# Kernel tuning notes

Hardware: AMD Instinct MI355X
Metric: run time of the kernel (lower is better)

## Reference

```python
import jax, jax.numpy as jnp
import numpy as np


def setup_inputs() -> dict:
    key = jax.random.key(0)
    ks = jax.random.split(key, 8)
    B, N, D, H = 8, 512, 64, 64
    user_embeddings = jax.random.normal(ks[0], (B, N, D), dtype=jnp.float32)
    past_lengths = jax.random.randint(ks[1], (B,), 0, N)
    valid_mask = jnp.ones((B, N), dtype=jnp.float32)
    # MLP params: Linear(4D -> H), PReLU (single slope), Linear(H -> 1)
    s1 = 1.0 / np.sqrt(4 * D)
    s2 = 1.0 / np.sqrt(H)
    W1 = jax.random.uniform(ks[2], (H, 4 * D), minval=-s1, maxval=s1, dtype=jnp.float32)
    b1 = jax.random.uniform(ks[3], (H,), minval=-s1, maxval=s1, dtype=jnp.float32)
    prelu_a = jnp.float32(0.25)
    W2 = jax.random.uniform(ks[4], (1, H), minval=-s2, maxval=s2, dtype=jnp.float32)
    b2 = jax.random.uniform(ks[5], (1,), minval=-s2, maxval=s2, dtype=jnp.float32)
    return {"past_lengths": past_lengths, "user_embeddings": user_embeddings,
            "valid_mask": valid_mask, "W1": W1, "b1": b1, "prelu_a": prelu_a,
            "W2": W2, "b2": b2}


def reference(past_lengths, user_embeddings, valid_mask, W1, b1, prelu_a, W2, b2):
    # DIN local activation attention with causal mask.
    # Original math: h = W1 @ concat(Q, K, Q-K, Q*K) + b1 per (q,k) pair.
    # Split W1 into its 4 D-sized blocks so the concat tensor [B,N,N,4D] is
    # never materialized; the pairwise hidden [B,N,N,H] is the only big buffer.
    B, N, D = user_embeddings.shape
    Wq, Wk, Wd, Wm = jnp.split(W1, 4, axis=1)  # each [H, D]
    x = user_embeddings
    # Q and (Q-K)'s +Q part -> per-query term; K and (Q-K)'s -K part -> per-key term
    hq = jnp.einsum('bqd,hd->bqh', x, Wq + Wd)          # [B,N,H]
    hk = jnp.einsum('bkd,hd->bkh', x, Wk - Wd)          # [B,N,H]
    hm = jnp.einsum('bqd,bkd,hd->bqkh', x, x, Wm)       # [B,N,N,H] (Q*K term)
    h = hq[:, :, None, :] + hk[:, None, :, :] + hm + b1
    h = jnp.where(h > 0, h, prelu_a * h)                # PReLU
    scores = jnp.einsum('bqkh,h->bqk', h, W2[0]) + b2[0]  # [B,N,N]
    causal = jnp.tril(jnp.ones((N, N), dtype=scores.dtype))
    scores = scores * causal[None, :, :]
    scores = scores * valid_mask[:, None, :]            # key-side padding mask
    encoded = jnp.einsum('bqk,bkd->bqd', scores, x)     # weighted sum (no softmax)
    return encoded
```

## Files before the change

### kernel.cpp

```cpp
#include <hip/hip_runtime.h>

#define NB 8
#define NN 512

#define WS_WMF  0
#define WS_WQDT 4096
#define WS_WKDT 8192
#define WS_HQ   12288
#define WS_BF   274432
#define WS_XT   536576

typedef float  fx4 __attribute__((ext_vector_type(4)));
typedef short  sx8 __attribute__((ext_vector_type(8)));

static __device__ inline unsigned short f2bf(float f) {
    unsigned int u = __float_as_uint(f);
    unsigned int r = (u + 0x7FFFu + ((u >> 16) & 1u)) >> 16;
    return (unsigned short)r;
}
static __device__ inline float bfl(unsigned int u) { return __uint_as_float(u << 16); }
static __device__ inline float bfh(unsigned int u) { return __uint_as_float(u & 0xFFFF0000u); }

__global__ __launch_bounds__(256) void pkA(const float* __restrict__ W1,
                                           float* __restrict__ ws) {
    int t = threadIdx.x;
    float* wqdT = ws + WS_WQDT;
    float* wkdT = ws + WS_WKDT;
    float* wmf  = ws + WS_WMF;
    for (int i = 0; i < 16; ++i) {
        int idx = t + i * 256;
        int h = idx >> 6, d = idx & 63;
        float wq = W1[h * 256 + d];
        float wk = W1[h * 256 + 64 + d];
        float wd = W1[h * 256 + 128 + d];
        wqdT[d * 64 + h] = wq + wd;
        wkdT[d * 64 + h] = wk - wd;
    }
    for (int i = 0; i < 2; ++i) {
        int e = t + i * 256;
        int slot = e >> 6, lane = e & 63;
        int ht = slot >> 1, hf = slot & 1;
        int m = lane & 15, qd = lane >> 4;
        int h = ht * 16 + m;
        int dbase = hf * 32 + qd * 8;
        #pragma unroll
        for (int j = 0; j < 8; ++j)
            wmf[e * 8 + j] = W1[h * 256 + 192 + dbase + j];
    }
}

__global__ __launch_bounds__(256) void pkB(const float* __restrict__ x,
                                           const float* __restrict__ b1,
                                           float* __restrict__ ws) {
    const float* wqdT = ws + WS_WQDT;
    const float* wkdT = ws + WS_WKDT;
    float* hq = ws + WS_HQ;
    unsigned short* bfp = (unsigned short*)(ws + WS_BF);
    __shared__ float xs[256];
    int t = threadIdx.x;
    int r0 = blockIdx.x * 4;
    xs[t] = x[r0 * 64 + t];
    __syncthreads();
    int r = t >> 6, h = t & 63;
    const float* xr = xs + r * 64;
    float aq = b1[h], ak = 0.f;
    #pragma unroll
    for (int d = 0; d < 64; ++d) {
        float xv = xr[d];
        aq += xv * wqdT[d * 64 + h];
        ak += xv * wkdT[d * 64 + h];
    }
    int row = r0 + r;
    hq[row * 64 + h] = aq;
    int bb = row >> 9, k = row & 511;
    int tt = k >> 4, nn = k & 15;
    int c  = 2 + (h >> 5);
    int qd = (h >> 3) & 3, j = h & 7;
    int ln = qd * 16 + nn;
    bfp[((((bb * 32 + tt) * 4 + c) * 64 + ln) << 3) + j] = f2bf(ak);
}

__global__ __launch_bounds__(128) void pkC(const float* __restrict__ x,
                                           float* __restrict__ ws) {
    unsigned short* bfp = (unsigned short*)(ws + WS_BF);
    int b = blockIdx.x >> 5, t5 = blockIdx.x & 31;
    int tid = threadIdx.x;
    int c = tid >> 6, L = tid & 63;
    int nn = L & 15, qd = L >> 4;
    const float* src = x + ((b * 512 + t5 * 16 + nn) * 64 + c * 32 + qd * 8);
    fx4 v0 = *(const fx4*)src;
    fx4 v1 = *(const fx4*)(src + 4);
    uint4 o;
    o.x = (unsigned)f2bf(v0[0]) | ((unsigned)f2bf(v0[1]) << 16);
    o.y = (unsigned)f2bf(v0[2]) | ((unsigned)f2bf(v0[3]) << 16);
    o.z = (unsigned)f2bf(v1[0]) | ((unsigned)f2bf(v1[1]) << 16);
    o.w = (unsigned)f2bf(v1[2]) | ((unsigned)f2bf(v1[3]) << 16);
    *(uint4*)(bfp + ((((b * 32 + t5) * 4 + c) * 64 + L) << 3)) = o;
}

__global__ __launch_bounds__(256) void pkD(const float* __restrict__ x,
                                           const float* __restrict__ vm,
                                           float* __restrict__ ws) {
    unsigned short* xtp = (unsigned short*)(ws + WS_XT);
    int b = blockIdx.x >> 5, t5 = blockIdx.x & 31;
    int tid = threadIdx.x;
    int d = tid >> 2;
    int kl0 = (tid & 3) * 4;
    unsigned short u[4];
    #pragma unroll
    for (int i = 0; i < 4; ++i) {
        int k = t5 * 16 + kl0 + i;
        float v = x[(b * 512 + k) * 64 + d] * vm[b * 512 + k];
        u[i] = f2bf(v);
    }
    uint2 o;
    o.x = (unsigned)u[0] | ((unsigned)u[1] << 16);
    o.y = (unsigned)u[2] | ((unsigned)u[3] << 16);
    *(uint2*)(xtp + (((b * 32 + t5) * 64 + d) * 16 + kl0)) = o;
}

__global__ __launch_bounds__(256) void k2_main(const float* __restrict__ x,
                                               const float* __restrict__ prelu_a,
                                               const float* __restrict__ W2,
                                               const float* __restrict__ b2,
                                               const float* __restrict__ ws,
                                               float* __restrict__ out) {
    const int tid  = threadIdx.x;
    const int lane = tid & 63;
    const int wid  = blockIdx.x * 4 + (tid >> 6);
    const int b    = wid >> 9;
    const int rr_  = wid & 511;
    const int q    = (rr_ & 1) ? (511 - (rr_ >> 1)) : (rr_ >> 1);
    const int n    = lane & 15, quad = lane >> 4;
    const int bq   = b * 512 + q;

    const float* wmf = ws + WS_WMF;
    const float* hq  = ws + WS_HQ;
    const unsigned short* bfp = (const unsigned short*)(ws + WS_BF);
    const unsigned short* xtp = (const unsigned short*)(ws + WS_XT);

    const float pa  = prelu_a[0];
    const float b2v = b2[0];

    float hqr[4][4], w2r[4][4];
    #pragma unroll
    for (int ht = 0; ht < 4; ++ht) {
        fx4 vh = *(const fx4*)(hq + bq * 64 + ht * 16 + quad * 4);
        fx4 vw = *(const fx4*)(W2 + ht * 16 + quad * 4);
        #pragma unroll
        for (int r = 0; r < 4; ++r) { hqr[ht][r] = vh[r]; w2r[ht][r] = vw[r]; }
    }

    float xq[2][8];
    {
        const float* xp = x + bq * 64 + quad * 8;
        fx4 t0 = *(const fx4*)xp;
        fx4 t1 = *(const fx4*)(xp + 4);
        fx4 t2 = *(const fx4*)(xp + 32);
        fx4 t3 = *(const fx4*)(xp + 36);
        #pragma unroll
        for (int j = 0; j < 4; ++j) {
            xq[0][j] = t0[j]; xq[0][4 + j] = t1[j];
            xq[1][j] = t2[j]; xq[1][4 + j] = t3[j];
        }
    }

    sx8 afrag[4][2];
    #pragma unroll
    for (int ht = 0; ht < 4; ++ht)
        #pragma unroll
        for (int hf = 0; hf < 2; ++hf) {
            const float* wp = wmf + (((ht * 2 + hf) * 64 + lane) << 3);
            fx4 w0 = *(const fx4*)wp;
            fx4 w1 = *(const fx4*)(wp + 4);
            sx8 a;
            #pragma unroll
            for (int j = 0; j < 4; ++j) {
                a[j]     = (short)f2bf(w0[j] * xq[hf][j]);
                a[4 + j] = (short)f2bf(w1[j] * xq[hf][4 + j]);
            }
            afrag[ht][hf] = a;
        }

    sx8 oh[4];
    #pragma unroll
    for (int ht = 0; ht < 4; ++ht) {
        sx8 a;
        #pragma unroll
        for (int j = 0; j < 8; ++j) {
            int hp = (ht >> 1) * 32 + quad * 8 + j;
            a[j] = (hp == ht * 16 + n) ? (short)0x3F80 : (short)0;
        }
        oh[ht] = a;
    }

    float enc = 0.f;
    const int tmax = q >> 4;
    for (int t = 0; t <= tmax; ++t) {
        const unsigned short* fb = bfp + ((((b * 32 + t) * 4) * 64 + lane) << 3);
        sx8 bf0 = *(const sx8*)(fb);
        sx8 bf1 = *(const sx8*)(fb + 512);
        sx8 bf2 = *(const sx8*)(fb + 1024);
        sx8 bf3 = *(const sx8*)(fb + 1536);

        fx4 acc[4];
        #pragma unroll
        for (int ht = 0; ht < 4; ++ht) acc[ht] = (fx4){0.f, 0.f, 0.f, 0.f};
        #pragma unroll
        for (int ht = 0; ht < 4; ++ht)
            acc[ht] = __builtin_amdgcn_mfma_f32_16x16x32_bf16(afrag[ht][0], bf0, acc[ht], 0, 0, 0);
        #pragma unroll
        for (int ht = 0; ht < 4; ++ht)
            acc[ht] = __builtin_amdgcn_mfma_f32_16x16x32_bf16(afrag[ht][1], bf1, acc[ht], 0, 0, 0);
        #pragma unroll
        for (int ht = 0; ht < 4; ++ht)
            acc[ht] = __builtin_amdgcn_mfma_f32_16x16x32_bf16(oh[ht], (ht < 2) ? bf2 : bf3, acc[ht], 0, 0, 0);

        float s = 0.f;
        #pragma unroll
        for (int ht = 0; ht < 4; ++ht)
            #pragma unroll
            for (int r = 0; r < 4; ++r) {
                float z = acc[ht][r] + hqr[ht][r];
                z = z > 0.f ? z : z * pa;
                s = fmaf(w2r[ht][r], z, s);
            }
        s += __shfl_xor(s, 16, 64);
        s += __shfl_xor(s, 32, 64);
        int kk = t * 16 + n;
        s = (kk <= q) ? (s + b2v) : 0.f;

        const uint4* px = (const uint4*)(xtp + (((b * 32 + t) * 64 + lane) << 4));
        uint4 xa = px[0], xb = px[1];
        float xv[16];
        xv[0]  = bfl(xa.x); xv[1]  = bfh(xa.x);
        xv[2]  = bfl(xa.y); xv[3]  = bfh(xa.y);
        xv[4]  = bfl(xa.z); xv[5]  = bfh(xa.z);
        xv[6]  = bfl(xa.w); xv[7]  = bfh(xa.w);
        xv[8]  = bfl(xb.x); xv[9]  = bfh(xb.x);
        xv[10] = bfl(xb.y); xv[11] = bfh(xb.y);
        xv[12] = bfl(xb.z); xv[13] = bfh(xb.z);
        xv[14] = bfl(xb.w); xv[15] = bfh(xb.w);
        #pragma unroll
        for (int j = 0; j < 16; ++j) {
            float sj = __uint_as_float(__builtin_amdgcn_readlane(__float_as_uint(s), j));
            enc = fmaf(sj, xv[j], enc);
        }
    }
    out[bq * 64 + lane] = enc;
}

extern "C" void kernel_launch(void* const* d_in, const int* in_sizes, int n_in,
                              void* d_out, int out_size, void* d_ws, size_t ws_size,
                              hipStream_t stream) {
    const float* x   = (const float*)d_in[1];
    const float* vmk = (const float*)d_in[2];
    const float* W1  = (const float*)d_in[3];
    const float* b1  = (const float*)d_in[4];
    const float* pa  = (const float*)d_in[5];
    const float* W2  = (const float*)d_in[6];
    const float* b2  = (const float*)d_in[7];
    float* ws  = (float*)d_ws;
    float* out = (float*)d_out;

    hipLaunchKernelGGL(pkA, dim3(1), dim3(256), 0, stream, W1, ws);
    hipLaunchKernelGGL(pkB, dim3(NB * NN / 4), dim3(256), 0, stream, x, b1, ws);
    hipLaunchKernelGGL(pkC, dim3(NB * 32), dim3(128), 0, stream, x, ws);
    hipLaunchKernelGGL(pkD, dim3(NB * 32), dim3(256), 0, stream, x, vmk, ws);
    hipLaunchKernelGGL(k2_main, dim3(NB * NN / 4), dim3(256), 0, stream,
                       x, pa, W2, b2, ws, out);
}
```

Baseline: 122.3 us.

## Fuse prep kernels into one and compute weighted sum via MFMA over 32-key chunks

Merges the four preprocessing kernels into a single prep launch. Each block recomputes the combined Wq+Wd and Wk-Wd weights into padded shared memory instead of reading them from a one-block kernel's output. The main kernel now handles 32 keys per iteration as two interleaved 16-key MFMA chains. The score-times-x accumulation moves from a 16-step readlane/FMA loop to bf16 MFMAs, with scores packed and redistributed via ds_bpermute. hq is preloaded into the accumulator and PReLU uses min/max, which adds bf16 rounding of scores and redundant weight loads per block.

```diff
diff --git a/kernel.cpp b/kernel.cpp
--- a/kernel.cpp
+++ b/kernel.cpp
@@ -3,41 +3,106 @@
 #define NB 8
 #define NN 512
 
-#define WS_WMF  0
-#define WS_WQDT 4096
-#define WS_WKDT 8192
-#define WS_HQ   12288
-#define WS_BF   274432
-#define WS_XT   536576
-
-typedef float  fx4 __attribute__((ext_vector_type(4)));
-typedef short  sx8 __attribute__((ext_vector_type(8)));
+#define WS_WMF 0
+#define WS_HQ  4096
+#define WS_BF  266240
+#define WS_XE  528384
+
+typedef float fx4 __attribute__((ext_vector_type(4)));
+typedef short sx8 __attribute__((ext_vector_type(8)));
+typedef int   ix4 __attribute__((ext_vector_type(4)));
 
 static __device__ inline unsigned short f2bf(float f) {
-    unsigned int u = __float_as_uint(f);
-    unsigned int r = (u + 0x7FFFu + ((u >> 16) & 1u)) >> 16;
-    return (unsigned short)r;
+    unsigned u = __float_as_uint(f);
+    return (unsigned short)((u + 0x7FFFu + ((u >> 16) & 1u)) >> 16);
 }
-static __device__ inline float bfl(unsigned int u) { return __uint_as_float(u << 16); }
-static __device__ inline float bfh(unsigned int u) { return __uint_as_float(u & 0xFFFF0000u); }
-
-__global__ __launch_bounds__(256) void pkA(const float* __restrict__ W1,
-                                           float* __restrict__ ws) {
-    int t = threadIdx.x;
-    float* wqdT = ws + WS_WQDT;
-    float* wkdT = ws + WS_WKDT;
-    float* wmf  = ws + WS_WMF;
-    for (int i = 0; i < 16; ++i) {
-        int idx = t + i * 256;
-        int h = idx >> 6, d = idx & 63;
-        float wq = W1[h * 256 + d];
-        float wk = W1[h * 256 + 64 + d];
-        float wd = W1[h * 256 + 128 + d];
-        wqdT[d * 64 + h] = wq + wd;
-        wkdT[d * 64 + h] = wk - wd;
-    }
-    for (int i = 0; i < 2; ++i) {
-        int e = t + i * 256;
+
+__global__ __launch_bounds__(256) void prep(const float* __restrict__ x,
+                                            const float* __restrict__ vm,
+                                            const float* __restrict__ W1,
+                                            const float* __restrict__ b1,
+                                            float* __restrict__ ws) {
+    __shared__ float lwq[64 * 65];
+    __shared__ float lwk[64 * 65];
+    __shared__ float xs[256];
+    const int t = threadIdx.x;
+    const int blk = blockIdx.x;
+
+    {
+        int d = t & 63, hb = t >> 6;
+        #pragma unroll 4
+        for (int i = 0; i < 16; ++i) {
+            int h = i * 4 + hb;
+            float a = W1[h * 256 + d];
+            float bb = W1[h * 256 + 64 + d];
+            float c = W1[h * 256 + 128 + d];
+            lwq[d * 65 + h] = a + c;
+            lwk[d * 65 + h] = bb - c;
+        }
+    }
+    const int r0 = blk * 4;
+    xs[t] = x[r0 * 64 + t];
+    __syncthreads();
+
+    {
+        int r = t >> 6, h = t & 63;
+        const float* xr = xs + r * 64;
+        float aq = b1[h], ak = 0.f;
+        #pragma unroll
+        for (int dd = 0; dd < 64; ++dd) {
+            float xv = xr[dd];
+            aq = fmaf(xv, lwq[dd * 65 + h], aq);
+            ak = fmaf(xv, lwk[dd * 65 + h], ak);
+        }
+        int row = r0 + r;
+        (ws + WS_HQ)[row * 64 + h] = aq;
+        unsigned short* bfp = (unsigned short*)(ws + WS_BF);
+        int bb = row >> 9, k = row & 511;
+        int tt = k >> 4, nn = k & 15;
+        int c = 2 + (h >> 5);
+        int qd = (h >> 3) & 3, j = h & 7;
+        int ln = qd * 16 + nn;
+        bfp[((((bb * 32 + tt) * 4 + c) * 64 + ln) << 3) + j] = f2bf(ak);
+    }
+
+    if (blk < 256) {
+        int b = blk >> 5, t5 = blk & 31;
+        if (t < 128) {
+            unsigned short* bfp = (unsigned short*)(ws + WS_BF);
+            int c = t >> 6, L = t & 63;
+            int nn = L & 15, qd = L >> 4;
+            const float* src = x + ((b * 512 + t5 * 16 + nn) * 64 + c * 32 + qd * 8);
+            fx4 v0 = *(const fx4*)src;
+            fx4 v1 = *(const fx4*)(src + 4);
+            uint4 o;
+            o.x = (unsigned)f2bf(v0[0]) | ((unsigned)f2bf(v0[1]) << 16);
+            o.y = (unsigned)f2bf(v0[2]) | ((unsigned)f2bf(v0[3]) << 16);
+            o.z = (unsigned)f2bf(v1[0]) | ((unsigned)f2bf(v1[1]) << 16);
+            o.w = (unsigned)f2bf(v1[2]) | ((unsigned)f2bf(v1[3]) << 16);
+            *(uint4*)(bfp + ((((b * 32 + t5) * 4 + c) * 64 + L) << 3)) = o;
+        }
+        {
+            unsigned short* xep = (unsigned short*)(ws + WS_XE);
+            int c32 = t5 >> 1, half = t5 & 1;
+            int nt = t >> 6, r = t & 63;
+            int L = half * 32 + (r & 31);
+            int j0 = (r >> 5) * 4;
+            int quad = L >> 4, nn = L & 15;
+            unsigned short u[4];
+            #pragma unroll
+            for (int i = 0; i < 4; ++i) {
+                int key = c32 * 32 + quad * 8 + j0 + i;
+                float v = x[(b * 512 + key) * 64 + nt * 16 + nn] * vm[b * 512 + key];
+                u[i] = f2bf(v);
+            }
+            uint2 o;
+            o.x = (unsigned)u[0] | ((unsigned)u[1] << 16);
+            o.y = (unsigned)u[2] | ((unsigned)u[3] << 16);
+            *(uint2*)(xep + (((((b * 16 + c32) * 4 + nt) * 64 + L) << 3) + j0)) = o;
+        }
+    } else if (blk < 258) {
+        float* wmf = ws + WS_WMF;
+        int e = (blk - 256) * 256 + t;
         int slot = e >> 6, lane = e & 63;
         int ht = slot >> 1, hf = slot & 1;
         int m = lane & 15, qd = lane >> 4;
@@ -49,95 +114,25 @@
     }
 }
 
-__global__ __launch_bounds__(256) void pkB(const float* __restrict__ x,
-                                           const float* __restrict__ b1,
-                                           float* __restrict__ ws) {
-    const float* wqdT = ws + WS_WQDT;
-    const float* wkdT = ws + WS_WKDT;
-    float* hq = ws + WS_HQ;
-    unsigned short* bfp = (unsigned short*)(ws + WS_BF);
-    __shared__ float xs[256];
-    int t = threadIdx.x;
-    int r0 = blockIdx.x * 4;
-    xs[t] = x[r0 * 64 + t];
-    __syncthreads();
-    int r = t >> 6, h = t & 63;
-    const float* xr = xs + r * 64;
-    float aq = b1[h], ak = 0.f;
-    #pragma unroll
-    for (int d = 0; d < 64; ++d) {
-        float xv = xr[d];
-        aq += xv * wqdT[d * 64 + h];
-        ak += xv * wkdT[d * 64 + h];
-    }
-    int row = r0 + r;
-    hq[row * 64 + h] = aq;
-    int bb = row >> 9, k = row & 511;
-    int tt = k >> 4, nn = k & 15;
-    int c  = 2 + (h >> 5);
-    int qd = (h >> 3) & 3, j = h & 7;
-    int ln = qd * 16 + nn;
-    bfp[((((bb * 32 + tt) * 4 + c) * 64 + ln) << 3) + j] = f2bf(ak);
-}
-
-__global__ __launch_bounds__(128) void pkC(const float* __restrict__ x,
-                                           float* __restrict__ ws) {
-    unsigned short* bfp = (unsigned short*)(ws + WS_BF);
-    int b = blockIdx.x >> 5, t5 = blockIdx.x & 31;
-    int tid = threadIdx.x;
-    int c = tid >> 6, L = tid & 63;
-    int nn = L & 15, qd = L >> 4;
-    const float* src = x + ((b * 512 + t5 * 16 + nn) * 64 + c * 32 + qd * 8);
-    fx4 v0 = *(const fx4*)src;
-    fx4 v1 = *(const fx4*)(src + 4);
-    uint4 o;
-    o.x = (unsigned)f2bf(v0[0]) | ((unsigned)f2bf(v0[1]) << 16);
-    o.y = (unsigned)f2bf(v0[2]) | ((unsigned)f2bf(v0[3]) << 16);
-    o.z = (unsigned)f2bf(v1[0]) | ((unsigned)f2bf(v1[1]) << 16);
-    o.w = (unsigned)f2bf(v1[2]) | ((unsigned)f2bf(v1[3]) << 16);
-    *(uint4*)(bfp + ((((b * 32 + t5) * 4 + c) * 64 + L) << 3)) = o;
-}
-
-__global__ __launch_bounds__(256) void pkD(const float* __restrict__ x,
-                                           const float* __restrict__ vm,
-                                           float* __restrict__ ws) {
-    unsigned short* xtp = (unsigned short*)(ws + WS_XT);
-    int b = blockIdx.x >> 5, t5 = blockIdx.x & 31;
-    int tid = threadIdx.x;
-    int d = tid >> 2;
-    int kl0 = (tid & 3) * 4;
-    unsigned short u[4];
-    #pragma unroll
-    for (int i = 0; i < 4; ++i) {
-        int k = t5 * 16 + kl0 + i;
-        float v = x[(b * 512 + k) * 64 + d] * vm[b * 512 + k];
-        u[i] = f2bf(v);
-    }
-    uint2 o;
-    o.x = (unsigned)u[0] | ((unsigned)u[1] << 16);
-    o.y = (unsigned)u[2] | ((unsigned)u[3] << 16);
-    *(uint2*)(xtp + (((b * 32 + t5) * 64 + d) * 16 + kl0)) = o;
-}
-
-__global__ __launch_bounds__(256) void k2_main(const float* __restrict__ x,
-                                               const float* __restrict__ prelu_a,
-                                               const float* __restrict__ W2,
-                                               const float* __restrict__ b2,
-                                               const float* __restrict__ ws,
-                                               float* __restrict__ out) {
+__global__ __launch_bounds__(256, 4) void k2_main(const float* __restrict__ x,
+                                                  const float* __restrict__ prelu_a,
+                                                  const float* __restrict__ W2,
+                                                  const float* __restrict__ b2,
+                                                  const float* __restrict__ ws,
+                                                  float* __restrict__ out) {
     const int tid  = threadIdx.x;
     const int lane = tid & 63;
     const int wid  = blockIdx.x * 4 + (tid >> 6);
     const int b    = wid >> 9;
-    const int rr_  = wid & 511;
-    const int q    = (rr_ & 1) ? (511 - (rr_ >> 1)) : (rr_ >> 1);
+    const int rr   = wid & 511;
+    const int q    = (rr & 1) ? (511 - (rr >> 1)) : (rr >> 1);
     const int n    = lane & 15, quad = lane >> 4;
     const int bq   = b * 512 + q;
 
     const float* wmf = ws + WS_WMF;
     const float* hq  = ws + WS_HQ;
     const unsigned short* bfp = (const unsigned short*)(ws + WS_BF);
-    const unsigned short* xtp = (const unsigned short*)(ws + WS_XT);
+    const unsigned short* xep = (const unsigned short*)(ws + WS_XE);
 
     const float pa  = prelu_a[0];
     const float b2v = b2[0];
@@ -194,60 +189,95 @@
         oh[ht] = a;
     }
 
-    float enc = 0.f;
-    const int tmax = q >> 4;
-    for (int t = 0; t <= tmax; ++t) {
-        const unsigned short* fb = bfp + ((((b * 32 + t) * 4) * 64 + lane) << 3);
-        sx8 bf0 = *(const sx8*)(fb);
-        sx8 bf1 = *(const sx8*)(fb + 512);
-        sx8 bf2 = *(const sx8*)(fb + 1024);
-        sx8 bf3 = *(const sx8*)(fb + 1536);
-
-        fx4 acc[4];
-        #pragma unroll
-        for (int ht = 0; ht < 4; ++ht) acc[ht] = (fx4){0.f, 0.f, 0.f, 0.f};
-        #pragma unroll
-        for (int ht = 0; ht < 4; ++ht)
-            acc[ht] = __builtin_amdgcn_mfma_f32_16x16x32_bf16(afrag[ht][0], bf0, acc[ht], 0, 0, 0);
-        #pragma unroll
-        for (int ht = 0; ht < 4; ++ht)
-            acc[ht] = __builtin_amdgcn_mfma_f32_16x16x32_bf16(afrag[ht][1], bf1, acc[ht], 0, 0, 0);
-        #pragma unroll
-        for (int ht = 0; ht < 4; ++ht)
-            acc[ht] = __builtin_amdgcn_mfma_f32_16x16x32_bf16(oh[ht], (ht < 2) ? bf2 : bf3, acc[ht], 0, 0, 0);
-
-        float s = 0.f;
+    int idxs[8];
+    #pragma unroll
+    for (int j = 0; j < 8; ++j) idxs[j] = ((quad * 8 + j) & 15) << 2;
+    const unsigned sel = (quad < 2) ? 0x05040100u : 0x07060302u;
+
+    fx4 eacc[4];
+    #pragma unroll
+    for (int nt = 0; nt < 4; ++nt) eacc[nt] = (fx4){0.f, 0.f, 0.f, 0.f};
+
+    const int cmax = q >> 5;
+    for (int c = 0; c <= cmax; ++c) {
+        const unsigned short* fb = bfp + ((((b * 32 + 2 * c) * 4) * 64 + lane) << 3);
+        sx8 fa0 = *(const sx8*)(fb);
+        sx8 fa1 = *(const sx8*)(fb + 512);
+        sx8 fa2 = *(const sx8*)(fb + 1024);
+        sx8 fa3 = *(const sx8*)(fb + 1536);
+        sx8 fb0 = *(const sx8*)(fb + 2048);
+        sx8 fb1 = *(const sx8*)(fb + 2560);
+        sx8 fb2 = *(const sx8*)(fb + 3072);
+        sx8 fb3 = *(const sx8*)(fb + 3584);
+        const unsigned short* fe = xep + ((((b * 16 + c) * 4) * 64 + lane) << 3);
+        sx8 e0 = *(const sx8*)(fe);
+        sx8 e1 = *(const sx8*)(fe + 512);
+        sx8 e2 = *(const sx8*)(fe + 1024);
+        sx8 e3 = *(const sx8*)(fe + 1536);
+
+        fx4 accA[4], accB[4];
+        #pragma unroll
+        for (int ht = 0; ht < 4; ++ht) {
+            accA[ht] = (fx4){hqr[ht][0], hqr[ht][1], hqr[ht][2], hqr[ht][3]};
+            accB[ht] = accA[ht];
+        }
+        #pragma unroll
+        for (int ht = 0; ht < 4; ++ht) {
+            accA[ht] = __builtin_amdgcn_mfma_f32_16x16x32_bf16(afrag[ht][0], fa0, accA[ht], 0, 0, 0);
+            accB[ht] = __builtin_amdgcn_mfma_f32_16x16x32_bf16(afrag[ht][0], fb0, accB[ht], 0, 0, 0);
+        }
+        #pragma unroll
+        for (int ht = 0; ht < 4; ++ht) {
+            accA[ht] = __builtin_amdgcn_mfma_f32_16x16x32_bf16(afrag[ht][1], fa1, accA[ht], 0, 0, 0);
+            accB[ht] = __builtin_amdgcn_mfma_f32_16x16x32_bf16(afrag[ht][1], fb1, accB[ht], 0, 0, 0);
+        }
+        #pragma unroll
+        for (int ht = 0; ht < 4; ++ht) {
+            accA[ht] = __builtin_amdgcn_mfma_f32_16x16x32_bf16(oh[ht], (ht < 2) ? fa2 : fa3, accA[ht], 0, 0, 0);
+            accB[ht] = __builtin_amdgcn_mfma_f32_16x16x32_bf16(oh[ht], (ht < 2) ? fb2 : fb3, accB[ht], 0, 0, 0);
+        }
+
+        float s0 = 0.f, s1 = 0.f;
         #pragma unroll
         for (int ht = 0; ht < 4; ++ht)
             #pragma unroll
             for (int r = 0; r < 4; ++r) {
-                float z = acc[ht][r] + hqr[ht][r];
-                z = z > 0.f ? z : z * pa;
-                s = fmaf(w2r[ht][r], z, s);
+                float za = accA[ht][r];
+                float zb = accB[ht][r];
+                s0 = fmaf(w2r[ht][r], fmaf(pa, fminf(za, 0.f), fmaxf(za, 0.f)), s0);
+                s1 = fmaf(w2r[ht][r], fmaf(pa, fminf(zb, 0.f), fmaxf(zb, 0.f)), s1);
             }
-        s += __shfl_xor(s, 16, 64);
-        s += __shfl_xor(s, 32, 64);
-        int kk = t * 16 + n;
-        s = (kk <= q) ? (s + b2v) : 0.f;
-
-        const uint4* px = (const uint4*)(xtp + (((b * 32 + t) * 64 + lane) << 4));
-        uint4 xa = px[0], xb = px[1];
-        float xv[16];
-        xv[0]  = bfl(xa.x); xv[1]  = bfh(xa.x);
-        xv[2]  = bfl(xa.y); xv[3]  = bfh(xa.y);
-        xv[4]  = bfl(xa.z); xv[5]  = bfh(xa.z);
-        xv[6]  = bfl(xa.w); xv[7]  = bfh(xa.w);
-        xv[8]  = bfl(xb.x); xv[9]  = bfh(xb.x);
-        xv[10] = bfl(xb.y); xv[11] = bfh(xb.y);
-        xv[12] = bfl(xb.z); xv[13] = bfh(xb.z);
-        xv[14] = bfl(xb.w); xv[15] = bfh(xb.w);
-        #pragma unroll
-        for (int j = 0; j < 16; ++j) {
-            float sj = __uint_as_float(__builtin_amdgcn_readlane(__float_as_uint(s), j));
-            enc = fmaf(sj, xv[j], enc);
-        }
-    }
-    out[bq * 64 + lane] = enc;
+        s0 += __shfl_xor(s0, 16, 64);
+        s0 += __shfl_xor(s0, 32, 64);
+        s1 += __shfl_xor(s1, 16, 64);
+        s1 += __shfl_xor(s1, 32, 64);
+        int k0 = c * 32 + n;
+        s0 = (k0 <= q)      ? s0 + b2v : 0.f;
+        s1 = (k0 + 16 <= q) ? s1 + b2v : 0.f;
+
+        unsigned packed = (unsigned)f2bf(s0) | ((unsigned)f2bf(s1) << 16);
+        int g[8];
+        #pragma unroll
+        for (int j = 0; j < 8; ++j)
+            g[j] = __builtin_amdgcn_ds_bpermute(idxs[j], (int)packed);
+        ix4 sw;
+        sw[0] = (int)__builtin_amdgcn_perm((unsigned)g[1], (unsigned)g[0], sel);
+        sw[1] = (int)__builtin_amdgcn_perm((unsigned)g[3], (unsigned)g[2], sel);
+        sw[2] = (int)__builtin_amdgcn_perm((unsigned)g[5], (unsigned)g[4], sel);
+        sw[3] = (int)__builtin_amdgcn_perm((unsigned)g[7], (unsigned)g[6], sel);
+        sx8 sfrag = __builtin_bit_cast(sx8, sw);
+
+        eacc[0] = __builtin_amdgcn_mfma_f32_16x16x32_bf16(sfrag, e0, eacc[0], 0, 0, 0);
+        eacc[1] = __builtin_amdgcn_mfma_f32_16x16x32_bf16(sfrag, e1, eacc[1], 0, 0, 0);
+        eacc[2] = __builtin_amdgcn_mfma_f32_16x16x32_bf16(sfrag, e2, eacc[2], 0, 0, 0);
+        eacc[3] = __builtin_amdgcn_mfma_f32_16x16x32_bf16(sfrag, e3, eacc[3], 0, 0, 0);
+    }
+
+    float ov = eacc[0][0];
+    if (quad == 1) ov = eacc[1][0];
+    if (quad == 2) ov = eacc[2][0];
+    if (quad == 3) ov = eacc[3][0];
+    out[bq * 64 + quad * 16 + n] = ov;
 }
 
 extern "C" void kernel_launch(void* const* d_in, const int* in_sizes, int n_in,
@@ -263,10 +293,8 @@
     float* ws  = (float*)d_ws;
     float* out = (float*)d_out;
 
-    hipLaunchKernelGGL(pkA, dim3(1), dim3(256), 0, stream, W1, ws);
-    hipLaunchKernelGGL(pkB, dim3(NB * NN / 4), dim3(256), 0, stream, x, b1, ws);
-    hipLaunchKernelGGL(pkC, dim3(NB * 32), dim3(128), 0, stream, x, ws);
-    hipLaunchKernelGGL(pkD, dim3(NB * 32), dim3(256), 0, stream, x, vmk, ws);
+    hipLaunchKernelGGL(prep, dim3(NB * NN / 4), dim3(256), 0, stream,
+                       x, vmk, W1, b1, ws);
     hipLaunchKernelGGL(k2_main, dim3(NB * NN / 4), dim3(256), 0, stream,
                        x, pa, W2, b2, ws, out);
 }
```

Measured after the change: 193.3 us. 1.58x slower.
